# Kernel optimization log

Hardware: AMD Instinct MI355X
Metric: run time of the kernel (lower is better)

The kernel has to match this reference:

```python
import jax, jax.numpy as jnp
import numpy as np

D_IN = 256
DIMS = 256


def setup_inputs() -> dict:
    key = jax.random.key(0)
    k1, k2, k3, k4, k5 = jax.random.split(key, 5)
    B, Tq, Tk = 4, 512, 512
    query = jax.random.normal(k1, (B, Tq, D_IN), dtype=jnp.float32)
    value = jax.random.normal(k2, (B, Tk, D_IN), dtype=jnp.float32)
    # Dense(dims, use_bias=False) kernels (glorot-like scale) and AdditiveAttention scale vector
    Wq = jax.random.normal(k3, (D_IN, DIMS), dtype=jnp.float32) / np.sqrt(D_IN)
    Wv = jax.random.normal(k4, (D_IN, DIMS), dtype=jnp.float32) / np.sqrt(D_IN)
    scale = jax.random.normal(k5, (DIMS,), dtype=jnp.float32)
    return {"query": query, "value": value, "Wq": Wq, "Wv": Wv, "scale": scale}


def reference(query, value, Wq, Wv, scale):
    # q_proj: [B,Tq,d], k_proj: [B,Tk,d]; attention value = RAW value tensor (as in source)
    q = jnp.einsum("bqi,id->bqd", query, Wq)
    k = jnp.einsum("bki,id->bkd", value, Wv)
    # Additive (Bahdanau) scores: [B,Tq,Tk] via broadcast tanh then reduce with scale
    scores = jnp.einsum("bqkd,d->bqk", jnp.tanh(q[:, :, None, :] + k[:, None, :, :]), scale)
    attn = jax.nn.softmax(scores, axis=-1)  # masks are all-ones -> no-op
    out = jnp.einsum("bqk,bki->bqi", attn, value)
    return out, attn
```

## Files before the change

### kernel.cpp

```cpp
#include <hip/hip_runtime.h>

#define LOG2E 1.4426950408889634f
#define TWO_LOG2E 2.885390081777927f

__device__ __forceinline__ float fast_exp2(float x) { return __builtin_amdgcn_exp2f(x); }
__device__ __forceinline__ float fast_rcp(float x)  { return __builtin_amdgcn_rcpf(x); }

__device__ __forceinline__ void term2(float s0, float s1, float qx, float qy,
                                      float kx, float ky, float& acc) {
    const float A = fmaf(qx, kx, 1.f);
    const float B = fmaf(qy, ky, 1.f);
    acc = fmaf(fmaf(s1, A, s0 * B), fast_rcp(A * B), acc);
}

__global__ __launch_bounds__(256) void proj_kernel(
    const float* __restrict__ query, const float* __restrict__ value,
    const float* __restrict__ Wq, const float* __restrict__ Wv,
    float* __restrict__ eq, float* __restrict__ ekT)
{
    __shared__ float in_lds[8 * 256];
    const int t = threadIdx.x;
    const int row0 = blockIdx.x * 8;
    const float* src; const float* W;
    if (row0 < 2048) { src = query + (size_t)row0 * 256; W = Wq; }
    else { src = value + (size_t)(row0 - 2048) * 256; W = Wv; }

    const float4* s4 = (const float4*)src;
    float4* l4 = (float4*)in_lds;
    l4[t] = s4[t];
    l4[t + 256] = s4[t + 256];
    __syncthreads();

    float acc[8];
#pragma unroll
    for (int r = 0; r < 8; ++r) acc[r] = 0.f;

    for (int d = 0; d < 256; d += 4) {
        const float w0 = W[(d + 0) * 256 + t];
        const float w1 = W[(d + 1) * 256 + t];
        const float w2 = W[(d + 2) * 256 + t];
        const float w3 = W[(d + 3) * 256 + t];
#pragma unroll
        for (int r = 0; r < 8; ++r) {
            const float4 v = *(const float4*)&in_lds[r * 256 + d];
            acc[r] = fmaf(v.x, w0, acc[r]);
            acc[r] = fmaf(v.y, w1, acc[r]);
            acc[r] = fmaf(v.z, w2, acc[r]);
            acc[r] = fmaf(v.w, w3, acc[r]);
        }
    }

    if (row0 < 2048) {
        float* dst = eq + (size_t)row0 * 256;
#pragma unroll
        for (int r = 0; r < 8; ++r) dst[r * 256 + t] = fast_exp2(acc[r] * TWO_LOG2E);
    } else {
        const int r0 = row0 - 2048;
        const int bb = r0 >> 9, kin = r0 & 511;
        float* dstT = ekT + (size_t)bb * 131072 + (size_t)t * 512 + kin;
        float4 v0, v1;
        v0.x = fast_exp2(acc[0] * TWO_LOG2E); v0.y = fast_exp2(acc[1] * TWO_LOG2E);
        v0.z = fast_exp2(acc[2] * TWO_LOG2E); v0.w = fast_exp2(acc[3] * TWO_LOG2E);
        v1.x = fast_exp2(acc[4] * TWO_LOG2E); v1.y = fast_exp2(acc[5] * TWO_LOG2E);
        v1.z = fast_exp2(acc[6] * TWO_LOG2E); v1.w = fast_exp2(acc[7] * TWO_LOG2E);
        *(float4*)dstT = v0;
        *(float4*)(dstT + 4) = v1;
    }
}

#define EQ_ST 260
#define SS_ST 520
__global__ __launch_bounds__(512, 2) void fused_kernel(
    const float* __restrict__ eq, const float* __restrict__ ekT,
    const float* __restrict__ scale, const float* __restrict__ value,
    float* __restrict__ attn, float* __restrict__ out)
{
    __shared__ float eq_lds[8 * EQ_ST];
    __shared__ float sc_lds[256];
    __shared__ float s_tile[8 * SS_ST];
    __shared__ float red[4 * 8 * 256];
    __shared__ float inv_lds[8];

    const int t = threadIdx.x;
    const int w = t >> 6, lane = t & 63;
    const int qg = w >> 2;
    const int kg = ((w & 3) << 6) + lane;
    const int k0 = 2 * kg;
    const int qt = blockIdx.x, b = blockIdx.y;
    const int q0 = qt * 8;

    {
        const int row = t >> 6, c = t & 63;
        const float4 v = ((const float4*)(eq + (size_t)(b * 512 + q0) * 256))[row * 64 + c];
        *(float4*)&eq_lds[row * EQ_ST + 4 * c] = v;
    }
    if (t < 256) sc_lds[t] = -2.f * scale[t];
    __syncthreads();

    const float* ekTb = ekT + (size_t)b * 131072;
    const float* q0r = &eq_lds[(4 * qg + 0) * EQ_ST];
    const float* q1r = &eq_lds[(4 * qg + 1) * EQ_ST];
    const float* q2r = &eq_lds[(4 * qg + 2) * EQ_ST];
    const float* q3r = &eq_lds[(4 * qg + 3) * EQ_ST];

    float a00 = 0.f, a01 = 0.f, a10 = 0.f, a11 = 0.f;
    float a20 = 0.f, a21 = 0.f, a30 = 0.f, a31 = 0.f;

    float4 sv  = *(const float4*)&sc_lds[0];
    float4 qv0 = *(const float4*)&q0r[0];
    float4 qv1 = *(const float4*)&q1r[0];
    float4 qv2 = *(const float4*)&q2r[0];
    float4 qv3 = *(const float4*)&q3r[0];
    float2 k0v = *(const float2*)&ekTb[(size_t)0 * 512 + k0];
    float2 k1v = *(const float2*)&ekTb[(size_t)1 * 512 + k0];
    float2 k2v = *(const float2*)&ekTb[(size_t)2 * 512 + k0];
    float2 k3v = *(const float2*)&ekTb[(size_t)3 * 512 + k0];

#pragma unroll 4
    for (int d = 0; d < 256; d += 4) {
        const float4 csv = sv, c0 = qv0, c1 = qv1, c2 = qv2, c3 = qv3;
        const float2 ck0 = k0v, ck1 = k1v, ck2 = k2v, ck3 = k3v;

        if (d < 252) {
            const int dn = d + 4;
            sv  = *(const float4*)&sc_lds[dn];
            qv0 = *(const float4*)&q0r[dn];
            qv1 = *(const float4*)&q1r[dn];
            qv2 = *(const float4*)&q2r[dn];
            qv3 = *(const float4*)&q3r[dn];
            k0v = *(const float2*)&ekTb[(size_t)(dn + 0) * 512 + k0];
            k1v = *(const float2*)&ekTb[(size_t)(dn + 1) * 512 + k0];
            k2v = *(const float2*)&ekTb[(size_t)(dn + 2) * 512 + k0];
            k3v = *(const float2*)&ekTb[(size_t)(dn + 3) * 512 + k0];
        }

        term2(csv.x, csv.y, c0.x, c0.y, ck0.x, ck1.x, a00);
        term2(csv.z, csv.w, c0.z, c0.w, ck2.x, ck3.x, a00);
        term2(csv.x, csv.y, c0.x, c0.y, ck0.y, ck1.y, a01);
        term2(csv.z, csv.w, c0.z, c0.w, ck2.y, ck3.y, a01);

        term2(csv.x, csv.y, c1.x, c1.y, ck0.x, ck1.x, a10);
        term2(csv.z, csv.w, c1.z, c1.w, ck2.x, ck3.x, a10);
        term2(csv.x, csv.y, c1.x, c1.y, ck0.y, ck1.y, a11);
        term2(csv.z, csv.w, c1.z, c1.w, ck2.y, ck3.y, a11);

        term2(csv.x, csv.y, c2.x, c2.y, ck0.x, ck1.x, a20);
        term2(csv.z, csv.w, c2.z, c2.w, ck2.x, ck3.x, a20);
        term2(csv.x, csv.y, c2.x, c2.y, ck0.y, ck1.y, a21);
        term2(csv.z, csv.w, c2.z, c2.w, ck2.y, ck3.y, a21);

        term2(csv.x, csv.y, c3.x, c3.y, ck0.x, ck1.x, a30);
        term2(csv.z, csv.w, c3.z, c3.w, ck2.x, ck3.x, a30);
        term2(csv.x, csv.y, c3.x, c3.y, ck0.y, ck1.y, a31);
        term2(csv.z, csv.w, c3.z, c3.w, ck2.y, ck3.y, a31);
    }

    *(float2*)&s_tile[(4 * qg + 0) * SS_ST + k0] = make_float2(a00, a01);
    *(float2*)&s_tile[(4 * qg + 1) * SS_ST + k0] = make_float2(a10, a11);
    *(float2*)&s_tile[(4 * qg + 2) * SS_ST + k0] = make_float2(a20, a21);
    *(float2*)&s_tile[(4 * qg + 3) * SS_ST + k0] = make_float2(a30, a31);
    __syncthreads();

    {
        float x[8];
        float m = -1e30f;
#pragma unroll
        for (int j = 0; j < 8; ++j) {
            x[j] = s_tile[w * SS_ST + 64 * j + lane];
            m = fmaxf(m, x[j]);
        }
#pragma unroll
        for (int off = 32; off; off >>= 1) m = fmaxf(m, __shfl_xor(m, off));

        float sum = 0.f;
#pragma unroll
        for (int j = 0; j < 8; ++j) { x[j] = fast_exp2((x[j] - m) * LOG2E); sum += x[j]; }
#pragma unroll
        for (int off = 32; off; off >>= 1) sum += __shfl_xor(sum, off);
        const float inv = fast_rcp(sum);

        float* arow = attn + (size_t)(b * 512 + q0 + w) * 512;
#pragma unroll
        for (int j = 0; j < 8; ++j) {
            s_tile[w * SS_ST + 64 * j + lane] = x[j];
            arow[64 * j + lane] = x[j] * inv;
        }
        if (lane == 0) inv_lds[w] = inv;
    }
    __syncthreads();

    float4 acc[8];
#pragma unroll
    for (int r = 0; r < 8; ++r) acc[r] = make_float4(0.f, 0.f, 0.f, 0.f);

    const float* vbase = value + (size_t)(b * 512 + 64 * w) * 256;
    for (int k4 = 0; k4 < 64; k4 += 4) {
        const float4 v0 = *(const float4*)&vbase[(k4 + 0) * 256 + lane * 4];
        const float4 v1 = *(const float4*)&vbase[(k4 + 1) * 256 + lane * 4];
        const float4 v2 = *(const float4*)&vbase[(k4 + 2) * 256 + lane * 4];
        const float4 v3 = *(const float4*)&vbase[(k4 + 3) * 256 + lane * 4];
#pragma unroll
        for (int r = 0; r < 8; ++r) {
            const float4 s4 = *(const float4*)&s_tile[r * SS_ST + 64 * w + k4];
            acc[r].x = fmaf(s4.x, v0.x, acc[r].x); acc[r].y = fmaf(s4.x, v0.y, acc[r].y);
            acc[r].z = fmaf(s4.x, v0.z, acc[r].z); acc[r].w = fmaf(s4.x, v0.w, acc[r].w);
            acc[r].x = fmaf(s4.y, v1.x, acc[r].x); acc[r].y = fmaf(s4.y, v1.y, acc[r].y);
            acc[r].z = fmaf(s4.y, v1.z, acc[r].z); acc[r].w = fmaf(s4.y, v1.w, acc[r].w);
            acc[r].x = fmaf(s4.z, v2.x, acc[r].x); acc[r].y = fmaf(s4.z, v2.y, acc[r].y);
            acc[r].z = fmaf(s4.z, v2.z, acc[r].z); acc[r].w = fmaf(s4.z, v2.w, acc[r].w);
            acc[r].x = fmaf(s4.w, v3.x, acc[r].x); acc[r].y = fmaf(s4.w, v3.y, acc[r].y);
            acc[r].z = fmaf(s4.w, v3.z, acc[r].z); acc[r].w = fmaf(s4.w, v3.w, acc[r].w);
        }
    }

    if (w >= 4) {
#pragma unroll
        for (int r = 0; r < 8; ++r)
            *(float4*)&red[((w - 4) * 8 + r) * 256 + lane * 4] = acc[r];
    }
    __syncthreads();
    if (w < 4) {
#pragma unroll
        for (int r = 0; r < 8; ++r) {
            const float4 o = *(const float4*)&red[(w * 8 + r) * 256 + lane * 4];
            acc[r].x += o.x; acc[r].y += o.y; acc[r].z += o.z; acc[r].w += o.w;
        }
    }
    __syncthreads();
    if (w >= 2 && w < 4) {
#pragma unroll
        for (int r = 0; r < 8; ++r)
            *(float4*)&red[((w - 2) * 8 + r) * 256 + lane * 4] = acc[r];
    }
    __syncthreads();
    if (w < 2) {
#pragma unroll
        for (int r = 0; r < 8; ++r) {
            const float4 o = *(const float4*)&red[(w * 8 + r) * 256 + lane * 4];
            acc[r].x += o.x; acc[r].y += o.y; acc[r].z += o.z; acc[r].w += o.w;
        }
    }
    __syncthreads();
    if (w == 1) {
#pragma unroll
        for (int r = 0; r < 8; ++r)
            *(float4*)&red[r * 256 + lane * 4] = acc[r];
    }
    __syncthreads();
    if (w == 0) {
#pragma unroll
        for (int r = 0; r < 8; ++r) {
            const float4 o = *(const float4*)&red[r * 256 + lane * 4];
            const float iv = inv_lds[r];
            float4 res;
            res.x = (acc[r].x + o.x) * iv;
            res.y = (acc[r].y + o.y) * iv;
            res.z = (acc[r].z + o.z) * iv;
            res.w = (acc[r].w + o.w) * iv;
            *(float4*)&out[(size_t)(b * 512 + q0 + r) * 256 + lane * 4] = res;
        }
    }
}

extern "C" void kernel_launch(void* const* d_in, const int* in_sizes, int n_in,
                              void* d_out, int out_size, void* d_ws, size_t ws_size,
                              hipStream_t stream) {
    const float* query = (const float*)d_in[0];
    const float* value = (const float*)d_in[1];
    const float* Wq    = (const float*)d_in[2];
    const float* Wv    = (const float*)d_in[3];
    const float* scale = (const float*)d_in[4];

    float* out0 = (float*)d_out;
    float* attn = out0 + 4 * 512 * 256;

    float* eq  = (float*)d_ws;
    float* ekT = eq + 2048 * 256;

    proj_kernel<<<512, 256, 0, stream>>>(query, value, Wq, Wv, eq, ekT);
    fused_kernel<<<dim3(64, 4), 512, 0, stream>>>(eq, ekT, scale, value, attn, out0);
}
```

Measured before the change: 63.70 us.

## Double fused-kernel block to 1024 threads splitting score d-range and value reduction

Raises the fused kernel block size from 512 to 1024 threads. Pairs of waves now split the 256-wide score reduction dimension in half and combine their partial scores through LDS. The PV stage splits keys into 32-row chunks across 16 waves, with an extra tree-reduction level. The aim is more parallelism per block, since the grid has only 256 blocks. The cost is an extra LDS read-modify-write with barriers, a much larger reduction buffer (64 KB), and launch bounds of (1024,4) that may squeeze registers.

Measured after the change: 126.0 us. 97.9% more time.

```diff
diff --git a/kernel.cpp b/kernel.cpp
--- a/kernel.cpp
+++ b/kernel.cpp
@@ -70,7 +70,7 @@
 
 #define EQ_ST 260
 #define SS_ST 520
-__global__ __launch_bounds__(512, 2) void fused_kernel(
+__global__ __launch_bounds__(1024, 4) void fused_kernel(
     const float* __restrict__ eq, const float* __restrict__ ekT,
     const float* __restrict__ scale, const float* __restrict__ value,
     float* __restrict__ attn, float* __restrict__ out)
@@ -78,23 +78,25 @@
     __shared__ float eq_lds[8 * EQ_ST];
     __shared__ float sc_lds[256];
     __shared__ float s_tile[8 * SS_ST];
-    __shared__ float red[4 * 8 * 256];
+    __shared__ float red[64 * 256];
     __shared__ float inv_lds[8];
 
     const int t = threadIdx.x;
     const int w = t >> 6, lane = t & 63;
-    const int qg = w >> 2;
-    const int kg = ((w & 3) << 6) + lane;
+    const int v = w >> 1, dh = w & 1;
+    const int qg = v >> 2;
+    const int kg = ((v & 3) << 6) + lane;
     const int k0 = 2 * kg;
     const int qt = blockIdx.x, b = blockIdx.y;
     const int q0 = qt * 8;
 
-    {
+    if (t < 512) {
         const int row = t >> 6, c = t & 63;
-        const float4 v = ((const float4*)(eq + (size_t)(b * 512 + q0) * 256))[row * 64 + c];
-        *(float4*)&eq_lds[row * EQ_ST + 4 * c] = v;
-    }
-    if (t < 256) sc_lds[t] = -2.f * scale[t];
+        const float4 vv = ((const float4*)(eq + (size_t)(b * 512 + q0) * 256))[t];
+        *(float4*)&eq_lds[row * EQ_ST + 4 * c] = vv;
+    } else if (t < 768) {
+        sc_lds[t - 512] = -2.f * scale[t - 512];
+    }
     __syncthreads();
 
     const float* ekTb = ekT + (size_t)b * 131072;
@@ -102,26 +104,27 @@
     const float* q1r = &eq_lds[(4 * qg + 1) * EQ_ST];
     const float* q2r = &eq_lds[(4 * qg + 2) * EQ_ST];
     const float* q3r = &eq_lds[(4 * qg + 3) * EQ_ST];
+    const int dlo = 128 * dh, dhi = dlo + 128;
 
     float a00 = 0.f, a01 = 0.f, a10 = 0.f, a11 = 0.f;
     float a20 = 0.f, a21 = 0.f, a30 = 0.f, a31 = 0.f;
 
-    float4 sv  = *(const float4*)&sc_lds[0];
-    float4 qv0 = *(const float4*)&q0r[0];
-    float4 qv1 = *(const float4*)&q1r[0];
-    float4 qv2 = *(const float4*)&q2r[0];
-    float4 qv3 = *(const float4*)&q3r[0];
-    float2 k0v = *(const float2*)&ekTb[(size_t)0 * 512 + k0];
-    float2 k1v = *(const float2*)&ekTb[(size_t)1 * 512 + k0];
-    float2 k2v = *(const float2*)&ekTb[(size_t)2 * 512 + k0];
-    float2 k3v = *(const float2*)&ekTb[(size_t)3 * 512 + k0];
+    float4 sv  = *(const float4*)&sc_lds[dlo];
+    float4 qv0 = *(const float4*)&q0r[dlo];
+    float4 qv1 = *(const float4*)&q1r[dlo];
+    float4 qv2 = *(const float4*)&q2r[dlo];
+    float4 qv3 = *(const float4*)&q3r[dlo];
+    float2 k0v = *(const float2*)&ekTb[(size_t)(dlo + 0) * 512 + k0];
+    float2 k1v = *(const float2*)&ekTb[(size_t)(dlo + 1) * 512 + k0];
+    float2 k2v = *(const float2*)&ekTb[(size_t)(dlo + 2) * 512 + k0];
+    float2 k3v = *(const float2*)&ekTb[(size_t)(dlo + 3) * 512 + k0];
 
 #pragma unroll 4
-    for (int d = 0; d < 256; d += 4) {
+    for (int d = dlo; d < dhi; d += 4) {
         const float4 csv = sv, c0 = qv0, c1 = qv1, c2 = qv2, c3 = qv3;
         const float2 ck0 = k0v, ck1 = k1v, ck2 = k2v, ck3 = k3v;
 
-        if (d < 252) {
+        if (d < dhi - 4) {
             const int dn = d + 4;
             sv  = *(const float4*)&sc_lds[dn];
             qv0 = *(const float4*)&q0r[dn];
@@ -155,13 +158,26 @@
         term2(csv.z, csv.w, c3.z, c3.w, ck2.y, ck3.y, a31);
     }
 
-    *(float2*)&s_tile[(4 * qg + 0) * SS_ST + k0] = make_float2(a00, a01);
-    *(float2*)&s_tile[(4 * qg + 1) * SS_ST + k0] = make_float2(a10, a11);
-    *(float2*)&s_tile[(4 * qg + 2) * SS_ST + k0] = make_float2(a20, a21);
-    *(float2*)&s_tile[(4 * qg + 3) * SS_ST + k0] = make_float2(a30, a31);
-    __syncthreads();
-
-    {
+    if (dh == 0) {
+        *(float2*)&s_tile[(4 * qg + 0) * SS_ST + k0] = make_float2(a00, a01);
+        *(float2*)&s_tile[(4 * qg + 1) * SS_ST + k0] = make_float2(a10, a11);
+        *(float2*)&s_tile[(4 * qg + 2) * SS_ST + k0] = make_float2(a20, a21);
+        *(float2*)&s_tile[(4 * qg + 3) * SS_ST + k0] = make_float2(a30, a31);
+    }
+    __syncthreads();
+    if (dh == 1) {
+        float2* p0 = (float2*)&s_tile[(4 * qg + 0) * SS_ST + k0];
+        float2* p1 = (float2*)&s_tile[(4 * qg + 1) * SS_ST + k0];
+        float2* p2 = (float2*)&s_tile[(4 * qg + 2) * SS_ST + k0];
+        float2* p3 = (float2*)&s_tile[(4 * qg + 3) * SS_ST + k0];
+        float2 t0 = *p0; t0.x += a00; t0.y += a01; *p0 = t0;
+        float2 t1 = *p1; t1.x += a10; t1.y += a11; *p1 = t1;
+        float2 t2 = *p2; t2.x += a20; t2.y += a21; *p2 = t2;
+        float2 t3 = *p3; t3.x += a30; t3.y += a31; *p3 = t3;
+    }
+    __syncthreads();
+
+    if (w < 8) {
         float x[8];
         float m = -1e30f;
 #pragma unroll
@@ -193,15 +209,15 @@
 #pragma unroll
     for (int r = 0; r < 8; ++r) acc[r] = make_float4(0.f, 0.f, 0.f, 0.f);
 
-    const float* vbase = value + (size_t)(b * 512 + 64 * w) * 256;
-    for (int k4 = 0; k4 < 64; k4 += 4) {
+    const float* vbase = value + (size_t)(b * 512 + 32 * w) * 256;
+    for (int k4 = 0; k4 < 32; k4 += 4) {
         const float4 v0 = *(const float4*)&vbase[(k4 + 0) * 256 + lane * 4];
         const float4 v1 = *(const float4*)&vbase[(k4 + 1) * 256 + lane * 4];
         const float4 v2 = *(const float4*)&vbase[(k4 + 2) * 256 + lane * 4];
         const float4 v3 = *(const float4*)&vbase[(k4 + 3) * 256 + lane * 4];
 #pragma unroll
         for (int r = 0; r < 8; ++r) {
-            const float4 s4 = *(const float4*)&s_tile[r * SS_ST + 64 * w + k4];
+            const float4 s4 = *(const float4*)&s_tile[r * SS_ST + 32 * w + k4];
             acc[r].x = fmaf(s4.x, v0.x, acc[r].x); acc[r].y = fmaf(s4.x, v0.y, acc[r].y);
             acc[r].z = fmaf(s4.x, v0.z, acc[r].z); acc[r].w = fmaf(s4.x, v0.w, acc[r].w);
             acc[r].x = fmaf(s4.y, v1.x, acc[r].x); acc[r].y = fmaf(s4.y, v1.y, acc[r].y);
@@ -213,7 +229,21 @@
         }
     }
 
-    if (w >= 4) {
+    if (w >= 8) {
+#pragma unroll
+        for (int r = 0; r < 8; ++r)
+            *(float4*)&red[((w - 8) * 8 + r) * 256 + lane * 4] = acc[r];
+    }
+    __syncthreads();
+    if (w < 8) {
+#pragma unroll
+        for (int r = 0; r < 8; ++r) {
+            const float4 o = *(const float4*)&red[(w * 8 + r) * 256 + lane * 4];
+            acc[r].x += o.x; acc[r].y += o.y; acc[r].z += o.z; acc[r].w += o.w;
+        }
+    }
+    __syncthreads();
+    if (w >= 4 && w < 8) {
 #pragma unroll
         for (int r = 0; r < 8; ++r)
             *(float4*)&red[((w - 4) * 8 + r) * 256 + lane * 4] = acc[r];
@@ -278,5 +308,5 @@
     float* ekT = eq + 2048 * 256;
 
     proj_kernel<<<512, 256, 0, stream>>>(query, value, Wq, Wv, eq, ekT);
-    fused_kernel<<<dim3(64, 4), 512, 0, stream>>>(eq, ekT, scale, value, attn, out0);
+    fused_kernel<<<dim3(64, 4), 1024, 0, stream>>>(eq, ekT, scale, value, attn, out0);
 }
```
